# Optimization experiments

Hardware: AMD Instinct MI355X
Metric: run time of the kernel (lower is better)

The kernel has to match this reference:

```python
import jax, jax.numpy as jnp
import numpy as np

EPS = 1e-5  # nn.RMSNorm eps


def setup_inputs() -> dict:
    key = jax.random.key(0)
    ks = jax.random.split(key, 8)
    B, L, D, R = 4, 4096, 2048, 4
    return {
        "h": jax.random.normal(ks[0], (B, L, D), jnp.float32),
        "h_o": jax.random.normal(ks[1], (B, L, D), jnp.float32),
        "static_alpha": jax.random.normal(ks[2], (R, R + 1), jnp.float32),
        "static_beta": jax.random.normal(ks[3], (R,), jnp.float32),
        "dynamic_alpha_fn": jax.random.normal(ks[4], (D, R + 1), jnp.float32) * 0.02,
        "dynamic_alpha_scale": jax.random.uniform(ks[5], (1,), jnp.float32, 0.005, 0.02),
        "dynamic_beta_fn": jax.random.normal(ks[6], (D,), jnp.float32) * 0.02,
        "dynamic_beta_scale": jnp.array([0.01], jnp.float32),
        "rms_weight": jax.random.uniform(ks[7], (D,), jnp.float32, 0.5, 1.5),
    }


def reference(h, h_o, static_alpha, static_beta, dynamic_alpha_fn,
              dynamic_alpha_scale, dynamic_beta_fn, dynamic_beta_scale,
              rms_weight):
    # RMSNorm over last dim with learnable weight (dynamic branch only)
    h_norm = h * jax.lax.rsqrt(jnp.mean(h * h, axis=-1, keepdims=True) + EPS) * rms_weight

    # dynamic alpha: [B,L,rate+1] offset broadcast against static [rate,rate+1]
    alpha_offset = jnp.tanh(h_norm @ dynamic_alpha_fn) * dynamic_alpha_scale  # [B,L,R+1]
    alpha = alpha_offset[:, :, None, :] + static_alpha                        # [B,L,R,R+1]

    # dynamic beta: scalar offset per token broadcast against static [rate]
    beta_offset = jnp.tanh(h_norm @ dynamic_beta_fn) * dynamic_beta_scale     # [B,L] * [1]
    beta = beta_offset[..., None] + static_beta                               # [B,L,R]

    # connect_width: mix_h[b,l,c,d] = sum_r alpha[b,l,r,c] * h[b,l,d]
    mix_h = jnp.einsum('blrc,bld->blcd', alpha, h)                            # [B,L,R+1,D]

    # connect_depth: broadcast outer product beta x h_o plus old streams, sum over rate
    out = jnp.sum(beta[..., None] * h_o[:, :, None, :] + mix_h[:, :, 1:, :], axis=2)
    return out  # [B,L,D]
```

## Files before the change

### kernel.cpp

```cpp
#include <hip/hip_runtime.h>
#include <math.h>


constexpr int D    = 2048;
constexpr int RATE = 4;
constexpr float EPS = 1e-5f;
constexpr int TPB  = 8;

__device__ __forceinline__ float fast_tanh(float x) {
    const float e = __expf(2.0f * x);
    return 1.0f - 2.0f / (e + 1.0f);
}

template<int CTRL>
__device__ __forceinline__ float dpp_add(float x) {
    int m = __builtin_amdgcn_update_dpp(0, __float_as_int(x), CTRL, 0xf, 0xf, true);
    return x + __int_as_float(m);
}

__device__ __forceinline__ float wave_sum_lane63(float x) {
    x = dpp_add<0x111>(x);
    x = dpp_add<0x112>(x);
    x = dpp_add<0x114>(x);
    x = dpp_add<0x118>(x);
    x = dpp_add<0x142>(x);
    x = dpp_add<0x143>(x);
    return x;
}

__global__ __launch_bounds__(256) void hyperconn_kernel(
    const float* __restrict__ h,
    const float* __restrict__ h_o,
    const float* __restrict__ sa,
    const float* __restrict__ sb,
    const float* __restrict__ fa,
    const float* __restrict__ a_sc,
    const float* __restrict__ fb,
    const float* __restrict__ b_sc,
    const float* __restrict__ w,
    float* __restrict__ out)
{
    const int tid  = threadIdx.x;
    const int d0   = tid * 8;
    const int wave = tid >> 6;
    const size_t t0 = (size_t)blockIdx.x * TPB;

    float4 hA[TPB], hB[TPB], oA[TPB], oB[TPB];
    #pragma unroll
    for (int i = 0; i < TPB; ++i) {
        const float* p = h + (t0 + i) * D + d0;
        hA[i] = *reinterpret_cast<const float4*>(p);
        hB[i] = *reinterpret_cast<const float4*>(p + 4);
    }
    #pragma unroll
    for (int i = 0; i < TPB; ++i) {
        const float* p = h_o + (t0 + i) * D + d0;
        oA[i] = *reinterpret_cast<const float4*>(p);
        oB[i] = *reinterpret_cast<const float4*>(p + 4);
    }

    float4 wa = *reinterpret_cast<const float4*>(w + d0);
    float4 wb = *reinterpret_cast<const float4*>(w + d0 + 4);
    const float wv[8] = {wa.x, wa.y, wa.z, wa.w, wb.x, wb.y, wb.z, wb.w};

    float fav[32];
    {
        float tmp[40];
        #pragma unroll
        for (int q = 0; q < 10; ++q) {
            float4 t = *reinterpret_cast<const float4*>(fa + (size_t)d0 * 5 + q * 4);
            tmp[q*4+0]=t.x; tmp[q*4+1]=t.y; tmp[q*4+2]=t.z; tmp[q*4+3]=t.w;
        }
        #pragma unroll
        for (int j = 0; j < 8; ++j)
            #pragma unroll
            for (int c = 0; c < 4; ++c)
                fav[j*4+c] = tmp[j*5 + 1 + c];
    }
    float4 fba = *reinterpret_cast<const float4*>(fb + d0);
    float4 fbb = *reinterpret_cast<const float4*>(fb + d0 + 4);
    const float fbv[8] = {fba.x, fba.y, fba.z, fba.w, fbb.x, fbb.y, fbb.z, fbb.w};

    const float a4 = a_sc[0] * (float)RATE;
    const float b4 = b_sc[0] * (float)RATE;
    float cs = 0.f;
    #pragma unroll
    for (int r = 0; r < RATE; ++r)
        #pragma unroll
        for (int c = 1; c <= RATE; ++c)
            cs += sa[r * (RATE + 1) + c];
    const float sbsum = sb[0] + sb[1] + sb[2] + sb[3];

    alignas(16) __shared__ float red[TPB][24];

    #pragma unroll
    for (int i = 0; i < TPB; ++i) {
        const float hv[8] = {hA[i].x, hA[i].y, hA[i].z, hA[i].w,
                             hB[i].x, hB[i].y, hB[i].z, hB[i].w};
        float acc[6] = {0.f, 0.f, 0.f, 0.f, 0.f, 0.f};
        #pragma unroll
        for (int j = 0; j < 8; ++j) {
            const float x  = hv[j];
            const float xw = x * wv[j];
            acc[0] = fmaf(x,  x,          acc[0]);
            acc[1] = fmaf(xw, fav[j*4+0], acc[1]);
            acc[2] = fmaf(xw, fav[j*4+1], acc[2]);
            acc[3] = fmaf(xw, fav[j*4+2], acc[3]);
            acc[4] = fmaf(xw, fav[j*4+3], acc[4]);
            acc[5] = fmaf(xw, fbv[j],     acc[5]);
        }
        #pragma unroll
        for (int k = 0; k < 6; ++k) acc[k] = wave_sum_lane63(acc[k]);
        if ((tid & 63) == 63) {
            #pragma unroll
            for (int k = 0; k < 6; ++k) red[i][wave * 6 + k] = acc[k];
        }
    }

    __syncthreads();

    #pragma unroll
    for (int i = 0; i < TPB; ++i) {
        const size_t base = (t0 + i) * D + d0;

        const float4 f0 = *reinterpret_cast<const float4*>(&red[i][0]);
        const float4 f1 = *reinterpret_cast<const float4*>(&red[i][4]);
        const float4 f2 = *reinterpret_cast<const float4*>(&red[i][8]);
        const float4 f3 = *reinterpret_cast<const float4*>(&red[i][12]);
        const float4 f4 = *reinterpret_cast<const float4*>(&red[i][16]);
        const float4 f5 = *reinterpret_cast<const float4*>(&red[i][20]);
        const float tot0 = f0.x + f1.z + f3.x + f4.z;
        const float tot1 = f0.y + f1.w + f3.y + f4.w;
        const float tot2 = f0.z + f2.x + f3.z + f5.x;
        const float tot3 = f0.w + f2.y + f3.w + f5.y;
        const float tot4 = f1.x + f2.z + f4.x + f5.z;
        const float tot5 = f1.y + f2.w + f4.y + f5.w;

        const float rms  = rsqrtf(tot0 * (1.0f / (float)D) + EPS);
        const float s_h  = a4 * (fast_tanh(tot1 * rms) + fast_tanh(tot2 * rms) +
                                 fast_tanh(tot3 * rms) + fast_tanh(tot4 * rms)) + cs;
        const float s_ho = b4 * fast_tanh(tot5 * rms) + sbsum;

        float4 r0, r1;
        r0.x = fmaf(s_ho, oA[i].x, s_h * hA[i].x);
        r0.y = fmaf(s_ho, oA[i].y, s_h * hA[i].y);
        r0.z = fmaf(s_ho, oA[i].z, s_h * hA[i].z);
        r0.w = fmaf(s_ho, oA[i].w, s_h * hA[i].w);
        r1.x = fmaf(s_ho, oB[i].x, s_h * hB[i].x);
        r1.y = fmaf(s_ho, oB[i].y, s_h * hB[i].y);
        r1.z = fmaf(s_ho, oB[i].z, s_h * hB[i].z);
        r1.w = fmaf(s_ho, oB[i].w, s_h * hB[i].w);
        *reinterpret_cast<float4*>(out + base)     = r0;
        *reinterpret_cast<float4*>(out + base + 4) = r1;
    }
}

extern "C" void kernel_launch(void* const* d_in, const int* in_sizes, int n_in,
                              void* d_out, int out_size, void* d_ws, size_t ws_size,
                              hipStream_t stream) {
    const float* h    = (const float*)d_in[0];
    const float* h_o  = (const float*)d_in[1];
    const float* sa   = (const float*)d_in[2];
    const float* sb   = (const float*)d_in[3];
    const float* fa   = (const float*)d_in[4];
    const float* a_sc = (const float*)d_in[5];
    const float* fb   = (const float*)d_in[6];
    const float* b_sc = (const float*)d_in[7];
    const float* w    = (const float*)d_in[8];
    float* out = (float*)d_out;

    const int ntok   = in_sizes[0] / D;
    const int blocks = ntok / TPB;
    hyperconn_kernel<<<blocks, 256, 0, stream>>>(h, h_o, sa, sb, fa, a_sc, fb, b_sc, w, out);
}
```

Before: 82.59 us.

## Use 512-thread blocks, drop register-held inputs, reload h in second pass

Doubles block size so each thread handles 4 elements instead of 8, and stops keeping all h and h_o rows in registers, reading h again in the output pass and loading h_o only there. The per-token scalars are now computed once by 8 threads and shared through LDS behind an extra barrier. The aim is to cut register pressure and raise occupancy (launch bounds request 6 blocks) for better latency hiding. The cost is a second read of h, which may hit in cache, plus one more sync.

```diff
diff --git a/kernel.cpp b/kernel.cpp
--- a/kernel.cpp
+++ b/kernel.cpp
@@ -6,6 +6,7 @@
 constexpr int RATE = 4;
 constexpr float EPS = 1e-5f;
 constexpr int TPB  = 8;
+constexpr int NT   = 512;
 
 __device__ __forceinline__ float fast_tanh(float x) {
     const float e = __expf(2.0f * x);
@@ -28,7 +29,7 @@
     return x;
 }
 
-__global__ __launch_bounds__(256) void hyperconn_kernel(
+__global__ __launch_bounds__(NT, 6) void hyperconn_kernel(
     const float* __restrict__ h,
     const float* __restrict__ h_o,
     const float* __restrict__ sa,
@@ -41,45 +42,28 @@
     float* __restrict__ out)
 {
     const int tid  = threadIdx.x;
-    const int d0   = tid * 8;
+    const int d0   = tid * 4;
     const int wave = tid >> 6;
     const size_t t0 = (size_t)blockIdx.x * TPB;
 
-    float4 hA[TPB], hB[TPB], oA[TPB], oB[TPB];
-    #pragma unroll
-    for (int i = 0; i < TPB; ++i) {
-        const float* p = h + (t0 + i) * D + d0;
-        hA[i] = *reinterpret_cast<const float4*>(p);
-        hB[i] = *reinterpret_cast<const float4*>(p + 4);
-    }
-    #pragma unroll
-    for (int i = 0; i < TPB; ++i) {
-        const float* p = h_o + (t0 + i) * D + d0;
-        oA[i] = *reinterpret_cast<const float4*>(p);
-        oB[i] = *reinterpret_cast<const float4*>(p + 4);
-    }
-
-    float4 wa = *reinterpret_cast<const float4*>(w + d0);
-    float4 wb = *reinterpret_cast<const float4*>(w + d0 + 4);
-    const float wv[8] = {wa.x, wa.y, wa.z, wa.w, wb.x, wb.y, wb.z, wb.w};
-
-    float fav[32];
+    const float4 wq  = *reinterpret_cast<const float4*>(w + d0);
+    const float wv[4] = {wq.x, wq.y, wq.z, wq.w};
+    float fav[16];
     {
-        float tmp[40];
+        float tmp[20];
         #pragma unroll
-        for (int q = 0; q < 10; ++q) {
+        for (int q = 0; q < 5; ++q) {
             float4 t = *reinterpret_cast<const float4*>(fa + (size_t)d0 * 5 + q * 4);
             tmp[q*4+0]=t.x; tmp[q*4+1]=t.y; tmp[q*4+2]=t.z; tmp[q*4+3]=t.w;
         }
         #pragma unroll
-        for (int j = 0; j < 8; ++j)
+        for (int j = 0; j < 4; ++j)
             #pragma unroll
             for (int c = 0; c < 4; ++c)
                 fav[j*4+c] = tmp[j*5 + 1 + c];
     }
-    float4 fba = *reinterpret_cast<const float4*>(fb + d0);
-    float4 fbb = *reinterpret_cast<const float4*>(fb + d0 + 4);
-    const float fbv[8] = {fba.x, fba.y, fba.z, fba.w, fbb.x, fbb.y, fbb.z, fbb.w};
+    const float4 fbq = *reinterpret_cast<const float4*>(fb + d0);
+    const float fbv[4] = {fbq.x, fbq.y, fbq.z, fbq.w};
 
     const float a4 = a_sc[0] * (float)RATE;
     const float b4 = b_sc[0] * (float)RATE;
@@ -91,15 +75,16 @@
             cs += sa[r * (RATE + 1) + c];
     const float sbsum = sb[0] + sb[1] + sb[2] + sb[3];
 
-    alignas(16) __shared__ float red[TPB][24];
+    __shared__ float  red[TPB][48];
+    __shared__ float2 s2[TPB];
 
     #pragma unroll
     for (int i = 0; i < TPB; ++i) {
-        const float hv[8] = {hA[i].x, hA[i].y, hA[i].z, hA[i].w,
-                             hB[i].x, hB[i].y, hB[i].z, hB[i].w};
+        const float4 hq = *reinterpret_cast<const float4*>(h + (t0 + i) * D + d0);
+        const float hv[4] = {hq.x, hq.y, hq.z, hq.w};
         float acc[6] = {0.f, 0.f, 0.f, 0.f, 0.f, 0.f};
         #pragma unroll
-        for (int j = 0; j < 8; ++j) {
+        for (int j = 0; j < 4; ++j) {
             const float x  = hv[j];
             const float xw = x * wv[j];
             acc[0] = fmaf(x,  x,          acc[0]);
@@ -119,39 +104,34 @@
 
     __syncthreads();
 
+    if (tid < TPB) {
+        float tot[6] = {0.f, 0.f, 0.f, 0.f, 0.f, 0.f};
+        #pragma unroll
+        for (int v = 0; v < 8; ++v)
+            #pragma unroll
+            for (int k = 0; k < 6; ++k)
+                tot[k] += red[tid][v * 6 + k];
+        const float rms  = rsqrtf(tot[0] * (1.0f / (float)D) + EPS);
+        const float s_h  = a4 * (fast_tanh(tot[1] * rms) + fast_tanh(tot[2] * rms) +
+                                 fast_tanh(tot[3] * rms) + fast_tanh(tot[4] * rms)) + cs;
+        const float s_ho = b4 * fast_tanh(tot[5] * rms) + sbsum;
+        s2[tid] = make_float2(s_h, s_ho);
+    }
+
+    __syncthreads();
+
     #pragma unroll
     for (int i = 0; i < TPB; ++i) {
+        const float2 s = s2[i];
         const size_t base = (t0 + i) * D + d0;
-
-        const float4 f0 = *reinterpret_cast<const float4*>(&red[i][0]);
-        const float4 f1 = *reinterpret_cast<const float4*>(&red[i][4]);
-        const float4 f2 = *reinterpret_cast<const float4*>(&red[i][8]);
-        const float4 f3 = *reinterpret_cast<const float4*>(&red[i][12]);
-        const float4 f4 = *reinterpret_cast<const float4*>(&red[i][16]);
-        const float4 f5 = *reinterpret_cast<const float4*>(&red[i][20]);
-        const float tot0 = f0.x + f1.z + f3.x + f4.z;
-        const float tot1 = f0.y + f1.w + f3.y + f4.w;
-        const float tot2 = f0.z + f2.x + f3.z + f5.x;
-        const float tot3 = f0.w + f2.y + f3.w + f5.y;
-        const float tot4 = f1.x + f2.z + f4.x + f5.z;
-        const float tot5 = f1.y + f2.w + f4.y + f5.w;
-
-        const float rms  = rsqrtf(tot0 * (1.0f / (float)D) + EPS);
-        const float s_h  = a4 * (fast_tanh(tot1 * rms) + fast_tanh(tot2 * rms) +
-                                 fast_tanh(tot3 * rms) + fast_tanh(tot4 * rms)) + cs;
-        const float s_ho = b4 * fast_tanh(tot5 * rms) + sbsum;
-
-        float4 r0, r1;
-        r0.x = fmaf(s_ho, oA[i].x, s_h * hA[i].x);
-        r0.y = fmaf(s_ho, oA[i].y, s_h * hA[i].y);
-        r0.z = fmaf(s_ho, oA[i].z, s_h * hA[i].z);
-        r0.w = fmaf(s_ho, oA[i].w, s_h * hA[i].w);
-        r1.x = fmaf(s_ho, oB[i].x, s_h * hB[i].x);
-        r1.y = fmaf(s_ho, oB[i].y, s_h * hB[i].y);
-        r1.z = fmaf(s_ho, oB[i].z, s_h * hB[i].z);
-        r1.w = fmaf(s_ho, oB[i].w, s_h * hB[i].w);
-        *reinterpret_cast<float4*>(out + base)     = r0;
-        *reinterpret_cast<float4*>(out + base + 4) = r1;
+        const float4 hq = *reinterpret_cast<const float4*>(h   + base);
+        const float4 oq = *reinterpret_cast<const float4*>(h_o + base);
+        float4 r;
+        r.x = fmaf(s.y, oq.x, s.x * hq.x);
+        r.y = fmaf(s.y, oq.y, s.x * hq.y);
+        r.z = fmaf(s.y, oq.z, s.x * hq.z);
+        r.w = fmaf(s.y, oq.w, s.x * hq.w);
+        *reinterpret_cast<float4*>(out + base) = r;
     }
 }
 
@@ -171,5 +151,5 @@
 
     const int ntok   = in_sizes[0] / D;
     const int blocks = ntok / TPB;
-    hyperconn_kernel<<<blocks, 256, 0, stream>>>(h, h_o, sa, sb, fa, a_sc, fb, b_sc, w, out);
+    hyperconn_kernel<<<blocks, NT, 0, stream>>>(h, h_o, sa, sb, fa, a_sc, fb, b_sc, w, out);
 }
```

Result: slower. 86.67 us (+4.9%).
